# Kernel optimization log

Measured on AMD Instinct MI355X. Metric: run time of the kernel, lower is better.

The kernel has to match this reference:

```python
import jax, jax.numpy as jnp
import numpy as np

IN_CH = 512
MID_CH = IN_CH // 8  # 64


def setup_inputs() -> dict:
    key = jax.random.key(0)
    ks = jax.random.split(key, 7)
    B, C, H, W = 8, IN_CH, 64, 64
    s = 1.0 / np.sqrt(C)
    x = jax.random.normal(ks[0], (B, C, H, W), dtype=jnp.float32)
    wq = jax.random.normal(ks[1], (MID_CH, C), dtype=jnp.float32) * s
    bq = jax.random.normal(ks[2], (MID_CH,), dtype=jnp.float32) * 0.01
    wk = jax.random.normal(ks[3], (MID_CH, C), dtype=jnp.float32) * s
    bk = jax.random.normal(ks[4], (MID_CH,), dtype=jnp.float32) * 0.01
    wv = jax.random.normal(ks[5], (C, C), dtype=jnp.float32) * s
    bv = jax.random.normal(ks[6], (C,), dtype=jnp.float32) * 0.01
    gamma = jnp.array([0.5], dtype=jnp.float32)
    return {"x": x, "wq": wq, "bq": bq, "wk": wk, "bk": bk,
            "wv": wv, "bv": bv, "gamma": gamma}


def reference(x, wq, bq, wk, bk, wv, bv, gamma):
    B, C, H, W = x.shape
    N = H * W
    xf = x.reshape(B, C, N)  # flatten spatial -> [B, C, N]
    # 1x1 convs are channel-wise matmuls
    q = jnp.einsum('mc,bcn->bnm', wq, xf) + bq  # [B, N, mid]
    k = jnp.einsum('mc,bcn->bmn', wk, xf) + bk[None, :, None]  # [B, mid, N]
    v = jnp.einsum('oc,bcn->bon', wv, xf) + bv[None, :, None]  # [B, C, N]
    sim = jnp.einsum('bnm,bmj->bnj', q, k)  # [B, N, N]
    sim = jax.nn.softmax(sim, axis=-1)
    # feat[b,c,i] = sum_j v[b,c,j] * sim[b,i,j]   (value @ sim^T)
    feat = jnp.einsum('bcj,bij->bci', v, sim).reshape(B, C, H, W)
    return gamma[0] * feat + x
```

## Files before the change

### kernel.cpp

```cpp
#include <hip/hip_runtime.h>
#include <hip/hip_bf16.h>


#define BB 8
#define CC 512
#define MM 64
#define NN 4096

typedef __attribute__((ext_vector_type(8))) short bf16x8;
typedef __attribute__((ext_vector_type(8))) _Float16 f16x8;
typedef __attribute__((ext_vector_type(4))) float f32x4;

__device__ unsigned g_kmax[BB];

__device__ __forceinline__ unsigned short f2bf(float f) {
  union { float f; unsigned u; } v; v.f = f;
  unsigned r = v.u + 0x7fffu + ((v.u >> 16) & 1u);
  return (unsigned short)(r >> 16);
}
__device__ __forceinline__ float bf2f(unsigned short h) {
  union { unsigned u; float f; } v; v.u = ((unsigned)h) << 16;
  return v.f;
}
__device__ __forceinline__ unsigned short f2h(float f) {
  union { _Float16 h; unsigned short u; } v; v.h = (_Float16)f;
  return v.u;
}

__global__ void k_init() {
  if (threadIdx.x < BB) g_kmax[threadIdx.x] = 0u;
}

__global__ __launch_bounds__(256) void k_transpose(const float* __restrict__ x,
                                                   unsigned short* __restrict__ xT) {
  __shared__ float tile[64][65];
  const int b = blockIdx.z, c0 = blockIdx.y * 64, n0 = blockIdx.x * 64;
  const int t = threadIdx.x;
  {
    const int nl = t & 63, cl0 = t >> 6;
    const float* xp = x + ((size_t)b * CC + c0) * NN + n0;
#pragma unroll
    for (int r = 0; r < 16; r++) {
      const int cl = cl0 + r * 4;
      tile[cl][nl] = xp[(size_t)cl * NN + nl];
    }
  }
  __syncthreads();
  {
    const int cl = t & 63, nl0 = t >> 6;
    unsigned short* xtp = xT + ((size_t)b * NN + n0) * CC + c0;
#pragma unroll
    for (int r = 0; r < 16; r++) {
      const int nl = nl0 + r * 4;
      xtp[(size_t)nl * CC + cl] = f2bf(tile[cl][nl]);
    }
  }
}

__global__ __launch_bounds__(256, 2) void k_qkproj(
    const unsigned short* __restrict__ xT,
    const float* __restrict__ wq, const float* __restrict__ bq,
    const float* __restrict__ wk, const float* __restrict__ bk,
    unsigned short* __restrict__ qf, unsigned short* __restrict__ kf) {
  __shared__ float ksl[4][8][16];
  const int b = blockIdx.x & 7;
  const int n0 = (blockIdx.x >> 3) * 128;
  const int t = threadIdx.x, w = t >> 6, l = t & 63, lr = l & 15, g = l >> 4;

  const float* wqp = wq + (size_t)(w * 16 + lr) * CC + g * 8;
  const float* wkp = wk + (size_t)(w * 16 + lr) * CC + g * 8;
  const unsigned short* xp = xT + ((size_t)b * NN + n0 + lr) * CC + g * 8;

  f32x4 qacc[8], kacc[8];
#pragma unroll
  for (int nf = 0; nf < 8; nf++) {
    qacc[nf] = f32x4{0.f, 0.f, 0.f, 0.f};
    kacc[nf] = f32x4{0.f, 0.f, 0.f, 0.f};
  }

  for (int cc = 0; cc < CC; cc += 32) {
    bf16x8 qhi8, qlo8, khi8, klo8;
    {
      const f32x4 a0 = *reinterpret_cast<const f32x4*>(wqp + cc);
      const f32x4 a1 = *reinterpret_cast<const f32x4*>(wqp + cc + 4);
      const f32x4 c0 = *reinterpret_cast<const f32x4*>(wkp + cc);
      const f32x4 c1 = *reinterpret_cast<const f32x4*>(wkp + cc + 4);
#pragma unroll
      for (int e = 0; e < 4; e++) {
        unsigned short h;
        h = f2bf(a0[e]); qhi8[e] = (short)h; qlo8[e] = (short)f2bf(a0[e] - bf2f(h));
        h = f2bf(a1[e]); qhi8[e + 4] = (short)h; qlo8[e + 4] = (short)f2bf(a1[e] - bf2f(h));
        h = f2bf(c0[e]); khi8[e] = (short)h; klo8[e] = (short)f2bf(c0[e] - bf2f(h));
        h = f2bf(c1[e]); khi8[e + 4] = (short)h; klo8[e + 4] = (short)f2bf(c1[e] - bf2f(h));
      }
    }
    bf16x8 xb[8];
#pragma unroll
    for (int nf = 0; nf < 8; nf++)
      xb[nf] = *reinterpret_cast<const bf16x8*>(xp + (size_t)nf * 16 * CC + cc);
#pragma unroll
    for (int nf = 0; nf < 8; nf++) {
      qacc[nf] = __builtin_amdgcn_mfma_f32_16x16x32_bf16(qhi8, xb[nf], qacc[nf], 0, 0, 0);
      qacc[nf] = __builtin_amdgcn_mfma_f32_16x16x32_bf16(qlo8, xb[nf], qacc[nf], 0, 0, 0);
      kacc[nf] = __builtin_amdgcn_mfma_f32_16x16x32_bf16(khi8, xb[nf], kacc[nf], 0, 0, 0);
      kacc[nf] = __builtin_amdgcn_mfma_f32_16x16x32_bf16(klo8, xb[nf], kacc[nf], 0, 0, 0);
    }
  }

  float bqv[4], bkv[4];
#pragma unroll
  for (int r = 0; r < 4; r++) {
    bqv[r] = bq[w * 16 + g * 4 + r];
    bkv[r] = bk[w * 16 + g * 4 + r];
  }
  float kssp[8];
#pragma unroll
  for (int nf = 0; nf < 8; nf++) {
    float ks2 = 0.f;
    unsigned short qh[4], kh[4];
#pragma unroll
    for (int r = 0; r < 4; r++) {
      const float qv = qacc[nf][r] + bqv[r];
      const float kv = kacc[nf][r] + bkv[r];
      qh[r] = f2h(qv); kh[r] = f2h(kv);
      ks2 += kv * kv;
    }
    kssp[nf] = ks2;
    const int n = n0 + nf * 16 + lr;
    const size_t base = ((size_t)b * NN + n) * MM + w * 16 + g * 4;
    *reinterpret_cast<ushort4*>(qf + base) = make_ushort4(qh[0], qh[1], qh[2], qh[3]);
    *reinterpret_cast<ushort4*>(kf + base) = make_ushort4(kh[0], kh[1], kh[2], kh[3]);
  }
#pragma unroll
  for (int nf = 0; nf < 8; nf++) {
    kssp[nf] += __shfl_xor(kssp[nf], 16);
    kssp[nf] += __shfl_xor(kssp[nf], 32);
  }
  if (l < 16) {
#pragma unroll
    for (int nf = 0; nf < 8; nf++) ksl[w][nf][lr] = kssp[nf];
  }
  __syncthreads();
  if (t < 128) {
    const int nf = (t & 63) >> 4 | ((t >> 6) << 2);
    const int lr2 = t & 15;
    float kn2 = ksl[0][nf][lr2] + ksl[1][nf][lr2] + ksl[2][nf][lr2] + ksl[3][nf][lr2];
#pragma unroll
    for (int d = 1; d < 64; d <<= 1) kn2 = fmaxf(kn2, __shfl_xor(kn2, d));
    if ((t & 63) == 0) atomicMax(&g_kmax[b], __float_as_uint(kn2));
  }
}

__global__ __launch_bounds__(256) void k_vproj(
    const unsigned short* __restrict__ xT, const float* __restrict__ wv,
    const float* __restrict__ bv, unsigned short* __restrict__ vbf) {
  const int b = blockIdx.z, c0 = blockIdx.y * 64, n0 = blockIdx.x * 128;
  const int t = threadIdx.x, w = t >> 6, l = t & 63, lr = l & 15, g = l >> 4;
  const int nbase = n0 + w * 32;
  f32x4 acc[4][2] = {};
  for (int ks = 0; ks < 16; ks++) {
    const int kk = ks * 32 + g * 8;
    bf16x8 bfr[2];
#pragma unroll
    for (int nf = 0; nf < 2; nf++) {
      const int n = nbase + nf * 16 + lr;
      bfr[nf] = *reinterpret_cast<const bf16x8*>(xT + ((size_t)b * NN + n) * CC + kk);
    }
#pragma unroll
    for (int cf = 0; cf < 4; cf++) {
      const int c = c0 + cf * 16 + lr;
      const float* wp = wv + (size_t)c * CC + kk;
      const f32x4 w0 = *reinterpret_cast<const f32x4*>(wp);
      const f32x4 w1 = *reinterpret_cast<const f32x4*>(wp + 4);
      bf16x8 af;
      af[0] = (short)f2bf(w0[0]); af[1] = (short)f2bf(w0[1]);
      af[2] = (short)f2bf(w0[2]); af[3] = (short)f2bf(w0[3]);
      af[4] = (short)f2bf(w1[0]); af[5] = (short)f2bf(w1[1]);
      af[6] = (short)f2bf(w1[2]); af[7] = (short)f2bf(w1[3]);
      acc[cf][0] = __builtin_amdgcn_mfma_f32_16x16x32_bf16(af, bfr[0], acc[cf][0], 0, 0, 0);
      acc[cf][1] = __builtin_amdgcn_mfma_f32_16x16x32_bf16(af, bfr[1], acc[cf][1], 0, 0, 0);
    }
  }
#pragma unroll
  for (int cf = 0; cf < 4; cf++) {
#pragma unroll
    for (int r = 0; r < 4; r++) {
      const int c = c0 + cf * 16 + g * 4 + r;
      const float bvv = bv[c];
#pragma unroll
      for (int nf = 0; nf < 2; nf++) {
        const int n = nbase + nf * 16 + lr;
        vbf[((size_t)b * CC + c) * NN + n] = f2bf(acc[cf][nf][r] + bvv);
      }
    }
  }
}

__global__ __launch_bounds__(512, 2) void k_attn(
    const unsigned short* __restrict__ qf, const unsigned short* __restrict__ kf,
    const unsigned short* __restrict__ vbf, const float* __restrict__ x,
    const float* __restrict__ gamma, float* __restrict__ out) {
  __shared__ unsigned short P_lds[2][128][64];
  __shared__ float l_red[8][4][16];
  const int b = blockIdx.x & 7;
  const int idx = blockIdx.x >> 3;
  const int i0 = (idx >> 1) * 128;
  const int ch = idx & 1;
  const int t = threadIdx.x, w = t >> 6, l = t & 63, lr = l & 15, g = l >> 4;
  const int jf = w & 3, ig = w >> 2;
  const int wc = ch * 256 + w * 32;

  f16x8 qF[4][2];
#pragma unroll
  for (int q = 0; q < 4; q++) {
    const int i = i0 + (ig * 4 + q) * 16 + lr;
#pragma unroll
    for (int ks = 0; ks < 2; ks++)
      qF[q][ks] = *reinterpret_cast<const f16x8*>(qf + ((size_t)b * NN + i) * MM + ks * 32 + g * 8);
  }
  float mhat[4];
  {
    const float kroot = sqrtf(__uint_as_float(g_kmax[b])) * 1.001f;
#pragma unroll
    for (int q = 0; q < 4; q++) {
      float ssq = 0.f;
#pragma unroll
      for (int ks = 0; ks < 2; ks++)
#pragma unroll
        for (int e = 0; e < 8; e++) {
          const float qv = (float)qF[q][ks][e];
          ssq += qv * qv;
        }
      ssq += __shfl_xor(ssq, 16);
      ssq += __shfl_xor(ssq, 32);
      mhat[q] = sqrtf(ssq) * kroot - 44.f;
    }
  }

  const unsigned short* kp = kf + ((size_t)b * NN + jf * 16 + lr) * MM + g * 8;
  const unsigned short* pv = vbf + ((size_t)b * CC + wc + lr) * NN + g * 8;

  f32x4 acc[2][8];
#pragma unroll
  for (int cf = 0; cf < 2; cf++)
#pragma unroll
    for (int i2 = 0; i2 < 8; i2++) acc[cf][i2] = f32x4{0.f, 0.f, 0.f, 0.f};
  float lsum[4] = {0.f, 0.f, 0.f, 0.f};

  f16x8 kF[2];
#pragma unroll
  for (int ks = 0; ks < 2; ks++)
    kF[ks] = *reinterpret_cast<const f16x8*>(kp + ks * 32);
  bf16x8 vr0[2][2], vr1[2][2];
#pragma unroll
  for (int ks = 0; ks < 2; ks++)
#pragma unroll
    for (int cf = 0; cf < 2; cf++)
      vr0[ks][cf] = *reinterpret_cast<const bf16x8*>(pv + (size_t)cf * (16 * NN) + ks * 32);

  unsigned short* const pbase = &P_lds[0][0][0];

  auto iter = [&](int jb, bf16x8 (&vcur)[2][2], bf16x8 (&vnext)[2][2]) {
    const int buf = (jb >> 6) & 1;
    const int jn = (jb + 64) & (NN - 1);
    unsigned short* pb = pbase + buf * (128 * 64);

    f32x4 sa[4];
#pragma unroll
    for (int q = 0; q < 4; q++) {
      sa[q] = __builtin_amdgcn_mfma_f32_16x16x32_f16(kF[0], qF[q][0],
                                                     f32x4{0.f, 0.f, 0.f, 0.f}, 0, 0, 0);
      sa[q] = __builtin_amdgcn_mfma_f32_16x16x32_f16(kF[1], qF[q][1], sa[q], 0, 0, 0);
    }
#pragma unroll
    for (int ks = 0; ks < 2; ks++)
      kF[ks] = *reinterpret_cast<const f16x8*>(kp + (size_t)jn * MM + ks * 32);
#pragma unroll
    for (int q = 0; q < 4; q++) {
      const float p0 = __expf(sa[q][0] - mhat[q]);
      const float p1 = __expf(sa[q][1] - mhat[q]);
      const float p2 = __expf(sa[q][2] - mhat[q]);
      const float p3 = __expf(sa[q][3] - mhat[q]);
      lsum[q] += (p0 + p1) + (p2 + p3);
      const int row = (ig * 4 + q) * 16 + lr;
      const int colb = jf * 32 + g * 8;
      *reinterpret_cast<ushort4*>(
          (char*)pb + (row << 7) + (colb ^ ((row & 7) << 4))) =
          make_ushort4(f2bf(p0), f2bf(p1), f2bf(p2), f2bf(p3));
    }

    __builtin_amdgcn_sched_barrier(0);
    asm volatile("s_waitcnt lgkmcnt(0)" ::: "memory");
    __builtin_amdgcn_s_barrier();
    __builtin_amdgcn_sched_barrier(0);

#pragma unroll
    for (int ks = 0; ks < 2; ks++)
#pragma unroll
      for (int cf = 0; cf < 2; cf++)
        vnext[ks][cf] = *reinterpret_cast<const bf16x8*>(
            pv + (size_t)cf * (16 * NN) + jn + ks * 32);

    __builtin_amdgcn_s_setprio(1);
#pragma unroll
    for (int ks = 0; ks < 2; ks++) {
#pragma unroll
      for (int i2 = 0; i2 < 8; i2++) {
        const int row = i2 * 16 + lr;
        const int colb = ks * 64 + g * 16;
        const bf16x8 pf = *reinterpret_cast<const bf16x8*>(
            (char*)pb + (row << 7) + (colb ^ ((row & 7) << 4)));
        acc[0][i2] = __builtin_amdgcn_mfma_f32_16x16x32_bf16(vcur[ks][0], pf, acc[0][i2], 0, 0, 0);
        acc[1][i2] = __builtin_amdgcn_mfma_f32_16x16x32_bf16(vcur[ks][1], pf, acc[1][i2], 0, 0, 0);
      }
    }
    __builtin_amdgcn_s_setprio(0);
  };

  for (int jb = 0; jb < NN; jb += 128) {
    iter(jb, vr0, vr1);
    iter(jb + 64, vr1, vr0);
  }

#pragma unroll
  for (int q = 0; q < 4; q++) {
    lsum[q] += __shfl_xor(lsum[q], 16);
    lsum[q] += __shfl_xor(lsum[q], 32);
  }
  __syncthreads();
  if (l < 16) {
#pragma unroll
    for (int q = 0; q < 4; q++) l_red[w][q][lr] = lsum[q];
  }
  __syncthreads();
  const float gm = gamma[0];
  float inv[8];
#pragma unroll
  for (int i2 = 0; i2 < 8; i2++) {
    const int ig2 = i2 >> 2, q = i2 & 3;
    inv[i2] = gm / (l_red[ig2 * 4 + 0][q][lr] + l_red[ig2 * 4 + 1][q][lr] +
                    l_red[ig2 * 4 + 2][q][lr] + l_red[ig2 * 4 + 3][q][lr]);
  }

#pragma unroll
  for (int cf = 0; cf < 2; cf++) {
#pragma unroll
    for (int r = 0; r < 4; r++) {
      const int c = wc + cf * 16 + g * 4 + r;
      const size_t rowo = ((size_t)b * CC + c) * NN;
#pragma unroll
      for (int i2 = 0; i2 < 8; i2++) {
        const int i = i0 + i2 * 16 + lr;
        out[rowo + i] = acc[cf][i2][r] * inv[i2] + x[rowo + i];
      }
    }
  }
}

extern "C" void kernel_launch(void* const* d_in, const int* in_sizes, int n_in,
                              void* d_out, int out_size, void* d_ws, size_t ws_size,
                              hipStream_t stream) {
  const float* x = (const float*)d_in[0];
  const float* wq = (const float*)d_in[1];
  const float* bq = (const float*)d_in[2];
  const float* wk = (const float*)d_in[3];
  const float* bk = (const float*)d_in[4];
  const float* wv = (const float*)d_in[5];
  const float* bv = (const float*)d_in[6];
  const float* gamma = (const float*)d_in[7];
  float* out = (float*)d_out;

  char* ws = (char*)d_ws;
  unsigned short* xT = (unsigned short*)(ws);
  unsigned short* vbf = (unsigned short*)(ws + 33554432);
  unsigned short* qfp = (unsigned short*)(ws + 67108864);
  unsigned short* kfp = (unsigned short*)(ws + 71303168);

  k_init<<<1, 64, 0, stream>>>();
  k_transpose<<<dim3(64, 8, 8), 256, 0, stream>>>(x, xT);
  k_qkproj<<<dim3(256), 256, 0, stream>>>(xT, wq, bq, wk, bk, qfp, kfp);
  k_vproj<<<dim3(32, 8, 8), 256, 0, stream>>>(xT, wv, bv, vbf);
  k_attn<<<dim3(512), 512, 0, stream>>>(qfp, kfp, vbf, x, gamma, out);
}
```

Measured before the change: 392.3 us.

## Precompute bf16 weights, merge projection kernels, software-pipeline attention loop with exp2

Adds a weight-conversion kernel that pre-splits wq/wk into bf16 hi/lo pairs and converts wv to bf16 once, so the projection kernels no longer convert weights per block. The QK and V projections become a single launch with smaller QK tiles. The attention loop is restructured so P for the next tile is written while the current tile's PV MFMAs run, with one barrier per step. Q is pre-scaled by log2(e) so exp2 replaces expf, and packed bf16 conversion instructions are used. The extra prologue and tail handling (vld guard) add complexity and risk of off-by-one in the pipelined loop.

```diff
diff --git a/kernel.cpp b/kernel.cpp
--- a/kernel.cpp
+++ b/kernel.cpp
@@ -6,6 +6,7 @@
 #define CC 512
 #define MM 64
 #define NN 4096
+#define LOG2E 1.4426950408889634f
 
 typedef __attribute__((ext_vector_type(8))) short bf16x8;
 typedef __attribute__((ext_vector_type(8))) _Float16 f16x8;
@@ -27,8 +28,22 @@
   return v.u;
 }
 
-__global__ void k_init() {
-  if (threadIdx.x < BB) g_kmax[threadIdx.x] = 0u;
+__global__ __launch_bounds__(256) void k_wconv(
+    const float* __restrict__ wq, const float* __restrict__ wk,
+    const float* __restrict__ wv,
+    unsigned short* __restrict__ wqhi, unsigned short* __restrict__ wqlo,
+    unsigned short* __restrict__ wkhi, unsigned short* __restrict__ wklo,
+    unsigned short* __restrict__ wvbf) {
+  const int tid = blockIdx.x * 256 + threadIdx.x;
+  if (tid < BB) g_kmax[tid] = 0u;
+  if (tid < MM * CC) {
+    float v = wq[tid];
+    unsigned short h = f2bf(v);
+    wqhi[tid] = h; wqlo[tid] = f2bf(v - bf2f(h));
+    v = wk[tid]; h = f2bf(v);
+    wkhi[tid] = h; wklo[tid] = f2bf(v - bf2f(h));
+  }
+  for (int i = tid; i < CC * CC; i += 65536) wvbf[i] = f2bf(wv[i]);
 }
 
 __global__ __launch_bounds__(256) void k_transpose(const float* __restrict__ x,
@@ -57,140 +72,126 @@
   }
 }
 
-__global__ __launch_bounds__(256, 2) void k_qkproj(
+__global__ __launch_bounds__(256, 2) void k_proj(
     const unsigned short* __restrict__ xT,
-    const float* __restrict__ wq, const float* __restrict__ bq,
-    const float* __restrict__ wk, const float* __restrict__ bk,
-    unsigned short* __restrict__ qf, unsigned short* __restrict__ kf) {
-  __shared__ float ksl[4][8][16];
-  const int b = blockIdx.x & 7;
-  const int n0 = (blockIdx.x >> 3) * 128;
+    const unsigned short* __restrict__ wqhi, const unsigned short* __restrict__ wqlo,
+    const unsigned short* __restrict__ wkhi, const unsigned short* __restrict__ wklo,
+    const float* __restrict__ bq, const float* __restrict__ bk,
+    const unsigned short* __restrict__ wvbf, const float* __restrict__ bv,
+    unsigned short* __restrict__ qf, unsigned short* __restrict__ kf,
+    unsigned short* __restrict__ vbf) {
+  __shared__ float ksl[4][4][16];
   const int t = threadIdx.x, w = t >> 6, l = t & 63, lr = l & 15, g = l >> 4;
 
-  const float* wqp = wq + (size_t)(w * 16 + lr) * CC + g * 8;
-  const float* wkp = wk + (size_t)(w * 16 + lr) * CC + g * 8;
-  const unsigned short* xp = xT + ((size_t)b * NN + n0 + lr) * CC + g * 8;
-
-  f32x4 qacc[8], kacc[8];
-#pragma unroll
-  for (int nf = 0; nf < 8; nf++) {
-    qacc[nf] = f32x4{0.f, 0.f, 0.f, 0.f};
-    kacc[nf] = f32x4{0.f, 0.f, 0.f, 0.f};
-  }
-
-  for (int cc = 0; cc < CC; cc += 32) {
-    bf16x8 qhi8, qlo8, khi8, klo8;
-    {
-      const f32x4 a0 = *reinterpret_cast<const f32x4*>(wqp + cc);
-      const f32x4 a1 = *reinterpret_cast<const f32x4*>(wqp + cc + 4);
-      const f32x4 c0 = *reinterpret_cast<const f32x4*>(wkp + cc);
-      const f32x4 c1 = *reinterpret_cast<const f32x4*>(wkp + cc + 4);
-#pragma unroll
-      for (int e = 0; e < 4; e++) {
-        unsigned short h;
-        h = f2bf(a0[e]); qhi8[e] = (short)h; qlo8[e] = (short)f2bf(a0[e] - bf2f(h));
-        h = f2bf(a1[e]); qhi8[e + 4] = (short)h; qlo8[e + 4] = (short)f2bf(a1[e] - bf2f(h));
-        h = f2bf(c0[e]); khi8[e] = (short)h; klo8[e] = (short)f2bf(c0[e] - bf2f(h));
-        h = f2bf(c1[e]); khi8[e + 4] = (short)h; klo8[e + 4] = (short)f2bf(c1[e] - bf2f(h));
-      }
-    }
-    bf16x8 xb[8];
-#pragma unroll
-    for (int nf = 0; nf < 8; nf++)
-      xb[nf] = *reinterpret_cast<const bf16x8*>(xp + (size_t)nf * 16 * CC + cc);
-#pragma unroll
-    for (int nf = 0; nf < 8; nf++) {
-      qacc[nf] = __builtin_amdgcn_mfma_f32_16x16x32_bf16(qhi8, xb[nf], qacc[nf], 0, 0, 0);
-      qacc[nf] = __builtin_amdgcn_mfma_f32_16x16x32_bf16(qlo8, xb[nf], qacc[nf], 0, 0, 0);
-      kacc[nf] = __builtin_amdgcn_mfma_f32_16x16x32_bf16(khi8, xb[nf], kacc[nf], 0, 0, 0);
-      kacc[nf] = __builtin_amdgcn_mfma_f32_16x16x32_bf16(klo8, xb[nf], kacc[nf], 0, 0, 0);
-    }
-  }
-
-  float bqv[4], bkv[4];
-#pragma unroll
-  for (int r = 0; r < 4; r++) {
-    bqv[r] = bq[w * 16 + g * 4 + r];
-    bkv[r] = bk[w * 16 + g * 4 + r];
-  }
-  float kssp[8];
-#pragma unroll
-  for (int nf = 0; nf < 8; nf++) {
-    float ks2 = 0.f;
-    unsigned short qh[4], kh[4];
+  if (blockIdx.x < 512) {
+    const int b = blockIdx.x & 7;
+    const int n0 = (blockIdx.x >> 3) * 64;
+    const unsigned short* qhp = wqhi + (size_t)(w * 16 + lr) * CC + g * 8;
+    const unsigned short* qlp = wqlo + (size_t)(w * 16 + lr) * CC + g * 8;
+    const unsigned short* khp = wkhi + (size_t)(w * 16 + lr) * CC + g * 8;
+    const unsigned short* klp = wklo + (size_t)(w * 16 + lr) * CC + g * 8;
+    const unsigned short* xp = xT + ((size_t)b * NN + n0 + lr) * CC + g * 8;
+    f32x4 qacc[4], kacc[4];
+#pragma unroll
+    for (int nf = 0; nf < 4; nf++) {
+      qacc[nf] = f32x4{0.f, 0.f, 0.f, 0.f};
+      kacc[nf] = f32x4{0.f, 0.f, 0.f, 0.f};
+    }
+    for (int cc = 0; cc < CC; cc += 32) {
+      const bf16x8 qh8 = *reinterpret_cast<const bf16x8*>(qhp + cc);
+      const bf16x8 ql8 = *reinterpret_cast<const bf16x8*>(qlp + cc);
+      const bf16x8 kh8 = *reinterpret_cast<const bf16x8*>(khp + cc);
+      const bf16x8 kl8 = *reinterpret_cast<const bf16x8*>(klp + cc);
+      bf16x8 xb[4];
+#pragma unroll
+      for (int nf = 0; nf < 4; nf++)
+        xb[nf] = *reinterpret_cast<const bf16x8*>(xp + (size_t)nf * 16 * CC + cc);
+#pragma unroll
+      for (int nf = 0; nf < 4; nf++) {
+        qacc[nf] = __builtin_amdgcn_mfma_f32_16x16x32_bf16(qh8, xb[nf], qacc[nf], 0, 0, 0);
+        qacc[nf] = __builtin_amdgcn_mfma_f32_16x16x32_bf16(ql8, xb[nf], qacc[nf], 0, 0, 0);
+        kacc[nf] = __builtin_amdgcn_mfma_f32_16x16x32_bf16(kh8, xb[nf], kacc[nf], 0, 0, 0);
+        kacc[nf] = __builtin_amdgcn_mfma_f32_16x16x32_bf16(kl8, xb[nf], kacc[nf], 0, 0, 0);
+      }
+    }
+    float bqv[4], bkv[4];
 #pragma unroll
     for (int r = 0; r < 4; r++) {
-      const float qv = qacc[nf][r] + bqv[r];
-      const float kv = kacc[nf][r] + bkv[r];
-      qh[r] = f2h(qv); kh[r] = f2h(kv);
-      ks2 += kv * kv;
-    }
-    kssp[nf] = ks2;
-    const int n = n0 + nf * 16 + lr;
-    const size_t base = ((size_t)b * NN + n) * MM + w * 16 + g * 4;
-    *reinterpret_cast<ushort4*>(qf + base) = make_ushort4(qh[0], qh[1], qh[2], qh[3]);
-    *reinterpret_cast<ushort4*>(kf + base) = make_ushort4(kh[0], kh[1], kh[2], kh[3]);
-  }
-#pragma unroll
-  for (int nf = 0; nf < 8; nf++) {
-    kssp[nf] += __shfl_xor(kssp[nf], 16);
-    kssp[nf] += __shfl_xor(kssp[nf], 32);
-  }
-  if (l < 16) {
-#pragma unroll
-    for (int nf = 0; nf < 8; nf++) ksl[w][nf][lr] = kssp[nf];
-  }
-  __syncthreads();
-  if (t < 128) {
-    const int nf = (t & 63) >> 4 | ((t >> 6) << 2);
-    const int lr2 = t & 15;
-    float kn2 = ksl[0][nf][lr2] + ksl[1][nf][lr2] + ksl[2][nf][lr2] + ksl[3][nf][lr2];
-#pragma unroll
-    for (int d = 1; d < 64; d <<= 1) kn2 = fmaxf(kn2, __shfl_xor(kn2, d));
-    if ((t & 63) == 0) atomicMax(&g_kmax[b], __float_as_uint(kn2));
-  }
-}
-
-__global__ __launch_bounds__(256) void k_vproj(
-    const unsigned short* __restrict__ xT, const float* __restrict__ wv,
-    const float* __restrict__ bv, unsigned short* __restrict__ vbf) {
-  const int b = blockIdx.z, c0 = blockIdx.y * 64, n0 = blockIdx.x * 128;
-  const int t = threadIdx.x, w = t >> 6, l = t & 63, lr = l & 15, g = l >> 4;
-  const int nbase = n0 + w * 32;
-  f32x4 acc[4][2] = {};
-  for (int ks = 0; ks < 16; ks++) {
-    const int kk = ks * 32 + g * 8;
-    bf16x8 bfr[2];
-#pragma unroll
-    for (int nf = 0; nf < 2; nf++) {
-      const int n = nbase + nf * 16 + lr;
-      bfr[nf] = *reinterpret_cast<const bf16x8*>(xT + ((size_t)b * NN + n) * CC + kk);
-    }
+      bqv[r] = bq[w * 16 + g * 4 + r];
+      bkv[r] = bk[w * 16 + g * 4 + r];
+    }
+    float kssp[4];
+#pragma unroll
+    for (int nf = 0; nf < 4; nf++) {
+      float ks2 = 0.f;
+      unsigned short qh[4], kh[4];
+#pragma unroll
+      for (int r = 0; r < 4; r++) {
+        const float qv = (qacc[nf][r] + bqv[r]) * LOG2E;
+        const float kv = kacc[nf][r] + bkv[r];
+        qh[r] = f2h(qv); kh[r] = f2h(kv);
+        ks2 += kv * kv;
+      }
+      kssp[nf] = ks2;
+      const int n = n0 + nf * 16 + lr;
+      const size_t base = ((size_t)b * NN + n) * MM + w * 16 + g * 4;
+      *reinterpret_cast<ushort4*>(qf + base) = make_ushort4(qh[0], qh[1], qh[2], qh[3]);
+      *reinterpret_cast<ushort4*>(kf + base) = make_ushort4(kh[0], kh[1], kh[2], kh[3]);
+    }
+#pragma unroll
+    for (int nf = 0; nf < 4; nf++) {
+      kssp[nf] += __shfl_xor(kssp[nf], 16);
+      kssp[nf] += __shfl_xor(kssp[nf], 32);
+    }
+    if (l < 16) {
+#pragma unroll
+      for (int nf = 0; nf < 4; nf++) ksl[w][nf][lr] = kssp[nf];
+    }
+    __syncthreads();
+    if (t < 64) {
+      const int nf2 = t >> 4, lr2 = t & 15;
+      float kn2 = ksl[0][nf2][lr2] + ksl[1][nf2][lr2] + ksl[2][nf2][lr2] + ksl[3][nf2][lr2];
+#pragma unroll
+      for (int d = 1; d < 64; d <<= 1) kn2 = fmaxf(kn2, __shfl_xor(kn2, d));
+      if (t == 0) atomicMax(&g_kmax[b], __float_as_uint(kn2));
+    }
+  } else {
+    const int blk = blockIdx.x - 512;
+    const int b = blk >> 8, c0 = ((blk >> 5) & 7) * 64, n0 = (blk & 31) * 128;
+    const int nbase = n0 + w * 32;
+    f32x4 acc[4][2];
 #pragma unroll
     for (int cf = 0; cf < 4; cf++) {
-      const int c = c0 + cf * 16 + lr;
-      const float* wp = wv + (size_t)c * CC + kk;
-      const f32x4 w0 = *reinterpret_cast<const f32x4*>(wp);
-      const f32x4 w1 = *reinterpret_cast<const f32x4*>(wp + 4);
-      bf16x8 af;
-      af[0] = (short)f2bf(w0[0]); af[1] = (short)f2bf(w0[1]);
-      af[2] = (short)f2bf(w0[2]); af[3] = (short)f2bf(w0[3]);
-      af[4] = (short)f2bf(w1[0]); af[5] = (short)f2bf(w1[1]);
-      af[6] = (short)f2bf(w1[2]); af[7] = (short)f2bf(w1[3]);
-      acc[cf][0] = __builtin_amdgcn_mfma_f32_16x16x32_bf16(af, bfr[0], acc[cf][0], 0, 0, 0);
-      acc[cf][1] = __builtin_amdgcn_mfma_f32_16x16x32_bf16(af, bfr[1], acc[cf][1], 0, 0, 0);
-    }
-  }
-#pragma unroll
-  for (int cf = 0; cf < 4; cf++) {
-#pragma unroll
-    for (int r = 0; r < 4; r++) {
-      const int c = c0 + cf * 16 + g * 4 + r;
-      const float bvv = bv[c];
+      acc[cf][0] = f32x4{0.f, 0.f, 0.f, 0.f};
+      acc[cf][1] = f32x4{0.f, 0.f, 0.f, 0.f};
+    }
+    for (int ks = 0; ks < 16; ks++) {
+      const int kk = ks * 32 + g * 8;
+      bf16x8 bfr[2];
 #pragma unroll
       for (int nf = 0; nf < 2; nf++) {
         const int n = nbase + nf * 16 + lr;
-        vbf[((size_t)b * CC + c) * NN + n] = f2bf(acc[cf][nf][r] + bvv);
+        bfr[nf] = *reinterpret_cast<const bf16x8*>(xT + ((size_t)b * NN + n) * CC + kk);
+      }
+#pragma unroll
+      for (int cf = 0; cf < 4; cf++) {
+        const bf16x8 af = *reinterpret_cast<const bf16x8*>(
+            wvbf + (size_t)(c0 + cf * 16 + lr) * CC + kk);
+        acc[cf][0] = __builtin_amdgcn_mfma_f32_16x16x32_bf16(af, bfr[0], acc[cf][0], 0, 0, 0);
+        acc[cf][1] = __builtin_amdgcn_mfma_f32_16x16x32_bf16(af, bfr[1], acc[cf][1], 0, 0, 0);
+      }
+    }
+#pragma unroll
+    for (int cf = 0; cf < 4; cf++) {
+#pragma unroll
+      for (int r = 0; r < 4; r++) {
+        const int c = c0 + cf * 16 + g * 4 + r;
+        const float bvv = bv[c];
+#pragma unroll
+        for (int nf = 0; nf < 2; nf++) {
+          const int n = nbase + nf * 16 + lr;
+          vbf[((size_t)b * CC + c) * NN + n] = f2bf(acc[cf][nf][r] + bvv);
+        }
       }
     }
   }
@@ -233,7 +234,7 @@
         }
       ssq += __shfl_xor(ssq, 16);
       ssq += __shfl_xor(ssq, 32);
-      mhat[q] = sqrtf(ssq) * kroot - 44.f;
+      mhat[q] = sqrtf(ssq) * kroot - 63.4786f;
     }
   }
 
@@ -247,79 +248,106 @@
     for (int i2 = 0; i2 < 8; i2++) acc[cf][i2] = f32x4{0.f, 0.f, 0.f, 0.f};
   float lsum[4] = {0.f, 0.f, 0.f, 0.f};
 
-  f16x8 kF[2];
+  char* const pbase = (char*)&P_lds[0][0][0];
+  int off_s[4];
+#pragma unroll
+  for (int q = 0; q < 4; q++) {
+    const int row = (ig * 4 + q) * 16 + lr;
+    off_s[q] = (row << 7) + ((jf * 32 + g * 8) ^ ((row & 7) << 4));
+  }
+
+  f16x8 kA[2], kB[2];
 #pragma unroll
   for (int ks = 0; ks < 2; ks++)
-    kF[ks] = *reinterpret_cast<const f16x8*>(kp + ks * 32);
-  bf16x8 vr0[2][2], vr1[2][2];
+    kA[ks] = *reinterpret_cast<const f16x8*>(kp + (size_t)ks * 32);
+  bf16x8 va[2][2], vb[2][2];
 #pragma unroll
   for (int ks = 0; ks < 2; ks++)
 #pragma unroll
     for (int cf = 0; cf < 2; cf++)
-      vr0[ks][cf] = *reinterpret_cast<const bf16x8*>(pv + (size_t)cf * (16 * NN) + ks * 32);
-
-  unsigned short* const pbase = &P_lds[0][0][0];
-
-  auto iter = [&](int jb, bf16x8 (&vcur)[2][2], bf16x8 (&vnext)[2][2]) {
-    const int buf = (jb >> 6) & 1;
-    const int jn = (jb + 64) & (NN - 1);
-    unsigned short* pb = pbase + buf * (128 * 64);
-
+      va[ks][cf] = *reinterpret_cast<const bf16x8*>(pv + (size_t)cf * (16 * NN) + ks * 32);
+#pragma unroll
+  for (int q = 0; q < 4; q++) {
+    f32x4 sa = __builtin_amdgcn_mfma_f32_16x16x32_f16(kA[0], qF[q][0],
+                                                      f32x4{0.f, 0.f, 0.f, 0.f}, 0, 0, 0);
+    sa = __builtin_amdgcn_mfma_f32_16x16x32_f16(kA[1], qF[q][1], sa, 0, 0, 0);
+    const float p0 = __builtin_amdgcn_exp2f(sa[0] - mhat[q]);
+    const float p1 = __builtin_amdgcn_exp2f(sa[1] - mhat[q]);
+    const float p2 = __builtin_amdgcn_exp2f(sa[2] - mhat[q]);
+    const float p3 = __builtin_amdgcn_exp2f(sa[3] - mhat[q]);
+    lsum[q] += (p0 + p1) + (p2 + p3);
+    unsigned r01, r23;
+    asm volatile("v_cvt_pk_bf16_f32 %0, %1, %2" : "=v"(r01) : "v"(p0), "v"(p1));
+    asm volatile("v_cvt_pk_bf16_f32 %0, %1, %2" : "=v"(r23) : "v"(p2), "v"(p3));
+    *reinterpret_cast<uint2*>(pbase + off_s[q]) = make_uint2(r01, r23);
+  }
+#pragma unroll
+  for (int ks = 0; ks < 2; ks++)
+    kB[ks] = *reinterpret_cast<const f16x8*>(kp + (size_t)64 * MM + ks * 32);
+  __builtin_amdgcn_sched_barrier(0);
+  asm volatile("s_waitcnt lgkmcnt(0)" ::: "memory");
+  __builtin_amdgcn_s_barrier();
+  __builtin_amdgcn_sched_barrier(0);
+
+  auto region = [&](int jb, bf16x8 (&vcur)[2][2], bf16x8 (&vnext)[2][2],
+                    f16x8 (&kuse)[2], f16x8 (&kpre)[2]) {
+    const int par = (jb >> 6) & 1;
+    const int j1 = (jb + 64) & (NN - 1);
+    const int j2 = (jb + 128) & (NN - 1);
+#pragma unroll
+    for (int ks = 0; ks < 2; ks++)
+#pragma unroll
+      for (int cf = 0; cf < 2; cf++)
+        vnext[ks][cf] = *reinterpret_cast<const bf16x8*>(
+            pv + (size_t)cf * (16 * NN) + j1 + ks * 32);
     f32x4 sa[4];
 #pragma unroll
     for (int q = 0; q < 4; q++) {
-      sa[q] = __builtin_amdgcn_mfma_f32_16x16x32_f16(kF[0], qF[q][0],
+      sa[q] = __builtin_amdgcn_mfma_f32_16x16x32_f16(kuse[0], qF[q][0],
                                                      f32x4{0.f, 0.f, 0.f, 0.f}, 0, 0, 0);
-      sa[q] = __builtin_amdgcn_mfma_f32_16x16x32_f16(kF[1], qF[q][1], sa[q], 0, 0, 0);
+      sa[q] = __builtin_amdgcn_mfma_f32_16x16x32_f16(kuse[1], qF[q][1], sa[q], 0, 0, 0);
     }
 #pragma unroll
     for (int ks = 0; ks < 2; ks++)
-      kF[ks] = *reinterpret_cast<const f16x8*>(kp + (size_t)jn * MM + ks * 32);
+      kpre[ks] = *reinterpret_cast<const f16x8*>(kp + (size_t)j2 * MM + ks * 32);
+    const bool vld = (jb + 64) < NN;
+    char* const pw = pbase + ((par ^ 1) << 14);
 #pragma unroll
     for (int q = 0; q < 4; q++) {
-      const float p0 = __expf(sa[q][0] - mhat[q]);
-      const float p1 = __expf(sa[q][1] - mhat[q]);
-      const float p2 = __expf(sa[q][2] - mhat[q]);
-      const float p3 = __expf(sa[q][3] - mhat[q]);
-      lsum[q] += (p0 + p1) + (p2 + p3);
-      const int row = (ig * 4 + q) * 16 + lr;
-      const int colb = jf * 32 + g * 8;
-      *reinterpret_cast<ushort4*>(
-          (char*)pb + (row << 7) + (colb ^ ((row & 7) << 4))) =
-          make_ushort4(f2bf(p0), f2bf(p1), f2bf(p2), f2bf(p3));
-    }
-
+      const float p0 = __builtin_amdgcn_exp2f(sa[q][0] - mhat[q]);
+      const float p1 = __builtin_amdgcn_exp2f(sa[q][1] - mhat[q]);
+      const float p2 = __builtin_amdgcn_exp2f(sa[q][2] - mhat[q]);
+      const float p3 = __builtin_amdgcn_exp2f(sa[q][3] - mhat[q]);
+      if (vld) lsum[q] += (p0 + p1) + (p2 + p3);
+      unsigned r01, r23;
+      asm volatile("v_cvt_pk_bf16_f32 %0, %1, %2" : "=v"(r01) : "v"(p0), "v"(p1));
+      asm volatile("v_cvt_pk_bf16_f32 %0, %1, %2" : "=v"(r23) : "v"(p2), "v"(p3));
+      *reinterpret_cast<uint2*>(pw + off_s[q]) = make_uint2(r01, r23);
+    }
+    char* const pr = pbase + (par << 14);
+    __builtin_amdgcn_s_setprio(1);
+#pragma unroll
+    for (int ks = 0; ks < 2; ks++) {
+#pragma unroll
+      for (int i2 = 0; i2 < 8; i2++) {
+        const int row = i2 * 16 + lr;
+        const int colb = ks * 64 + g * 16;
+        const bf16x8 pf = *reinterpret_cast<const bf16x8*>(
+            pr + (row << 7) + (colb ^ ((row & 7) << 4)));
+        acc[0][i2] = __builtin_amdgcn_mfma_f32_16x16x32_bf16(vcur[ks][0], pf, acc[0][i2], 0, 0, 0);
+        acc[1][i2] = __builtin_amdgcn_mfma_f32_16x16x32_bf16(vcur[ks][1], pf, acc[1][i2], 0, 0, 0);
+      }
+    }
+    __builtin_amdgcn_s_setprio(0);
     __builtin_amdgcn_sched_barrier(0);
     asm volatile("s_waitcnt lgkmcnt(0)" ::: "memory");
     __builtin_amdgcn_s_barrier();
     __builtin_amdgcn_sched_barrier(0);
-
-#pragma unroll
-    for (int ks = 0; ks < 2; ks++)
-#pragma unroll
-      for (int cf = 0; cf < 2; cf++)
-        vnext[ks][cf] = *reinterpret_cast<const bf16x8*>(
-            pv + (size_t)cf * (16 * NN) + jn + ks * 32);
-
-    __builtin_amdgcn_s_setprio(1);
-#pragma unroll
-    for (int ks = 0; ks < 2; ks++) {
-#pragma unroll
-      for (int i2 = 0; i2 < 8; i2++) {
-        const int row = i2 * 16 + lr;
-        const int colb = ks * 64 + g * 16;
-        const bf16x8 pf = *reinterpret_cast<const bf16x8*>(
-            (char*)pb + (row << 7) + (colb ^ ((row & 7) << 4)));
-        acc[0][i2] = __builtin_amdgcn_mfma_f32_16x16x32_bf16(vcur[ks][0], pf, acc[0][i2], 0, 0, 0);
-        acc[1][i2] = __builtin_amdgcn_mfma_f32_16x16x32_bf16(vcur[ks][1], pf, acc[1][i2], 0, 0, 0);
-      }
-    }
-    __builtin_amdgcn_s_setprio(0);
   };
 
-  for (int jb = 0; jb < NN; jb += 128) {
-    iter(jb, vr0, vr1);
-    iter(jb + 64, vr1, vr0);
+  for (int tt = 0; tt < 32; tt++) {
+    region(tt * 128, va, vb, kB, kA);
+    region(tt * 128 + 64, vb, va, kA, kB);
   }
 
 #pragma unroll
@@ -375,10 +403,15 @@
   unsigned short* vbf = (unsigned short*)(ws + 33554432);
   unsigned short* qfp = (unsigned short*)(ws + 67108864);
   unsigned short* kfp = (unsigned short*)(ws + 71303168);
-
-  k_init<<<1, 64, 0, stream>>>();
+  unsigned short* wqhi = (unsigned short*)(ws + 75497472);
+  unsigned short* wqlo = (unsigned short*)(ws + 75563008);
+  unsigned short* wkhi = (unsigned short*)(ws + 75628544);
+  unsigned short* wklo = (unsigned short*)(ws + 75694080);
+  unsigned short* wvbf = (unsigned short*)(ws + 75759616);
+
+  k_wconv<<<256, 256, 0, stream>>>(wq, wk, wv, wqhi, wqlo, wkhi, wklo, wvbf);
   k_transpose<<<dim3(64, 8, 8), 256, 0, stream>>>(x, xT);
-  k_qkproj<<<dim3(256), 256, 0, stream>>>(xT, wq, bq, wk, bk, qfp, kfp);
-  k_vproj<<<dim3(32, 8, 8), 256, 0, stream>>>(xT, wv, bv, vbf);
+  k_proj<<<2560, 256, 0, stream>>>(xT, wqhi, wqlo, wkhi, wklo, bq, bk, wvbf, bv,
+                                   qfp, kfp, vbf);
   k_attn<<<dim3(512), 512, 0, stream>>>(qfp, kfp, vbf, x, gamma, out);
 }
```

After: 335.6 us. 1.17x faster.
